# Optimization experiments

Hardware: AMD Instinct MI355X
Metric: run time of the kernel (lower is better)

The kernel has to match this reference:

```python
import math
import jax, jax.numpy as jnp
import numpy as np

B, S, D, H, F, L = 32, 512, 512, 8, 2048, 4
DH = D // H
ALPHA = 1.0
LN_EPS = 1e-12


def setup_inputs() -> dict:
    key = jax.random.key(0)
    ks = jax.random.split(key, 24)
    n = jax.random.normal
    inp = {
        "hidden_states": n(ks[0], (B, S, D), dtype=jnp.float32),
        "position_bias": n(ks[1], (1, H, S, S), dtype=jnp.float32) * 0.02,
        "timestamp": jnp.sort(jax.random.randint(ks[2], (B, S), 0, 10_000_000), axis=-1).astype(jnp.int64),
        # per-layer stacked BERT params
        "Wq": n(ks[3], (L, D, D), dtype=jnp.float32) * 0.02,
        "bq": jnp.zeros((L, D), dtype=jnp.float32),
        "Wk": n(ks[4], (L, D, D), dtype=jnp.float32) * 0.02,
        "bk": jnp.zeros((L, D), dtype=jnp.float32),
        "Wv": n(ks[5], (L, D, D), dtype=jnp.float32) * 0.02,
        "bv": jnp.zeros((L, D), dtype=jnp.float32),
        "Wo": n(ks[6], (L, D, D), dtype=jnp.float32) * 0.02,
        "bo": jnp.zeros((L, D), dtype=jnp.float32),
        "ln1_g": jnp.ones((L, D), dtype=jnp.float32),
        "ln1_b": jnp.zeros((L, D), dtype=jnp.float32),
        "Wi": n(ks[7], (L, D, F), dtype=jnp.float32) * 0.02,
        "bi": jnp.zeros((L, F), dtype=jnp.float32),
        "Wf": n(ks[8], (L, F, D), dtype=jnp.float32) * 0.02,
        "bf": jnp.zeros((L, D), dtype=jnp.float32),
        "ln2_g": jnp.ones((L, D), dtype=jnp.float32),
        "ln2_b": jnp.zeros((L, D), dtype=jnp.float32),
    }
    return inp


def _layernorm(x, g, b):
    mu = jnp.mean(x, axis=-1, keepdims=True)
    var = jnp.mean(jnp.square(x - mu), axis=-1, keepdims=True)
    return (x - mu) * jax.lax.rsqrt(var + LN_EPS) * g + b


def _encoder(hidden_states, position_bias, timestamp,
             Wq, bq, Wk, bk, Wv, bv, Wo, bo, ln1_g, ln1_b,
             Wi, bi, Wf, bf, ln2_g, ln2_b):
    b_, s_, d_ = hidden_states.shape
    # lag-time scale (encoder path: raw timestamps, minutes)
    t = timestamp.astype(jnp.float32)
    lag = (t[:, :, None] - t[:, None, :]) / (60.0 * 1000.0)  # [B,S,S]
    scale = (math.sqrt(DH) - ALPHA / (jnp.maximum(lag, 0.0) + 1.0) + ALPHA)[:, None, :, :]  # [B,1,S,S]

    x = hidden_states
    for l in range(L):
        q = (x @ Wq[l] + bq[l]).reshape(b_, s_, H, DH)
        k = (x @ Wk[l] + bk[l]).reshape(b_, s_, H, DH)
        v = (x @ Wv[l] + bv[l]).reshape(b_, s_, H, DH)
        scores = jnp.einsum('bqhd,bkhd->bhqk', q, k) / scale + position_bias
        probs = jax.nn.softmax(scores, axis=-1)
        ctx = jnp.einsum('bhqk,bkhd->bqhd', probs, v).reshape(b_, s_, d_)
        attn = _layernorm(ctx @ Wo[l] + bo[l] + x, ln1_g[l], ln1_b[l])
        h = jax.nn.gelu(attn @ Wi[l] + bi[l], approximate=False)
        x = _layernorm(h @ Wf[l] + bf[l] + attn, ln2_g[l], ln2_b[l])
    return x


def reference(hidden_states, position_bias, timestamp,
              Wq, bq, Wk, bk, Wv, bv, Wo, bo, ln1_g, ln1_b,
              Wi, bi, Wf, bf, ln2_g, ln2_b):
    return _encoder(hidden_states, position_bias, timestamp,
                    Wq, bq, Wk, bk, Wv, bv, Wo, bo, ln1_g, ln1_b,
                    Wi, bi, Wf, bf, ln2_g, ln2_b)
```

## Files before the change

kernel.cpp:

```cpp
#include <hip/hip_runtime.h>
#include <stdint.h>

#define B_ 32
#define S_ 512
#define D_ 512
#define H_ 8
#define F_ 2048
#define L_ 4
#define DH_ 64
#define M_ (B_*S_)

typedef unsigned short u16;
typedef float f32x4 __attribute__((ext_vector_type(4)));
typedef short bf16x8 __attribute__((ext_vector_type(8)));

__device__ __forceinline__ u16 f2b(float f) {
  unsigned u = __float_as_uint(f);
  u += 0x7FFFu + ((u >> 16) & 1u);
  return (u16)(u >> 16);
}
__device__ __forceinline__ float b2f(u16 u) {
  return __uint_as_float((unsigned)u << 16);
}
__device__ __forceinline__ void gld16(const void* g, void* l) {
  __builtin_amdgcn_global_load_lds((__attribute__((address_space(1))) void*)(void*)g,
                                   (__attribute__((address_space(3))) void*)l, 16, 0, 0);
}
__device__ __forceinline__ f32x4 mfma16(bf16x8 a, bf16x8 b, f32x4 c) {
  return __builtin_amdgcn_mfma_f32_16x16x32_bf16(a, b, c, 0, 0, 0);
}
__device__ __forceinline__ float gelu_fast(float x) {
  float z = 0.7978845608028654f * fmaf(0.044715f * x, x * x, x);
  float e = __expf(2.0f * z);
  float t = 1.0f - 2.0f * __builtin_amdgcn_rcpf(e + 1.0f);
  return 0.5f * x * (1.0f + t);
}

__global__ __launch_bounds__(256) void transpose_w(const float* __restrict__ in,
                                                   u16* __restrict__ out, int R, int C) {
  __shared__ float tile[32][33];
  const int l = blockIdx.z;
  in  += (size_t)l * R * C;
  out += (size_t)l * R * C;
  const int c0 = blockIdx.x * 32, r0 = blockIdx.y * 32;
  const int tx = threadIdx.x, ty = threadIdx.y;
#pragma unroll
  for (int k = 0; k < 4; k++)
    tile[ty + 8*k][tx] = in[(size_t)(r0 + ty + 8*k) * C + c0 + tx];
  __syncthreads();
#pragma unroll
  for (int k = 0; k < 4; k++)
    out[(size_t)(c0 + ty + 8*k) * R + r0 + tx] = f2b(tile[tx][ty + 8*k]);
}

__global__ __launch_bounds__(256) void prep_x(const float* __restrict__ h,
                                              u16* __restrict__ xb) {
  int i = blockIdx.x * 256 + threadIdx.x;
  float4 v = ((const float4*)h)[i];
  ushort4 u; u.x = f2b(v.x); u.y = f2b(v.y); u.z = f2b(v.z); u.w = f2b(v.w);
  ((ushort4*)xb)[i] = u;
}

__global__ __launch_bounds__(256) void prep_pb(const float* __restrict__ pb,
                                               u16* __restrict__ out) {
  int i = blockIdx.x * 256 + threadIdx.x;
  float4 v = ((const float4*)pb)[i];
  ushort4 o; o.x = f2b(v.x); o.y = f2b(v.y); o.z = f2b(v.z); o.w = f2b(v.w);
  ((ushort4*)out)[i] = o;
}

__device__ __forceinline__ void gemm_core(
    const u16* __restrict__ A, const u16* __restrict__ BT,
    const int N, const int K,
    const float* __restrict__ bias, u16* __restrict__ outb, const int epi)
{
  __shared__ u16 As[128*64];
  __shared__ u16 Bs[128*64];
  const int tid = threadIdx.x;
  const int wid = tid >> 6, lane = tid & 63;
  const int wm = (wid >> 1) * 64, wn = (wid & 1) * 64;
  const int lr = lane & 15, quad = lane >> 4;
  const int m0 = blockIdx.x * 128, n0 = blockIdx.y * 128;
  const int l7 = lane & 7, l3 = lane >> 3;
  const int cc = (l7 ^ l3) * 8;
  const int f8 = lr & 7;

  f32x4 acc[4][4];
#pragma unroll
  for (int i = 0; i < 4; i++)
#pragma unroll
    for (int j = 0; j < 4; j++) acc[i][j] = (f32x4){0.f, 0.f, 0.f, 0.f};

  const u16* Ag = A  + (size_t)(m0 + wid*16 + l3)*K + cc;
  const u16* Bg = BT + (size_t)(n0 + wid*16 + l3)*K + cc;
  u16* AsW = As + wid*1024;
  u16* BsW = Bs + wid*1024;

  for (int k0 = 0; k0 < K; k0 += 64) {
    gld16(Ag + k0,                 AsW);
    gld16(Ag + (size_t)8*K + k0,   AsW + 512);
    gld16(Ag + (size_t)64*K + k0,  AsW + 4096);
    gld16(Ag + (size_t)72*K + k0,  AsW + 4608);
    gld16(Bg + k0,                 BsW);
    gld16(Bg + (size_t)8*K + k0,   BsW + 512);
    gld16(Bg + (size_t)64*K + k0,  BsW + 4096);
    gld16(Bg + (size_t)72*K + k0,  BsW + 4608);
    __syncthreads();
#pragma unroll
    for (int kh = 0; kh < 2; kh++) {
      bf16x8 af[4], bfr[4];
#pragma unroll
      for (int i = 0; i < 4; i++)
        af[i]  = *(const bf16x8*)(As + (wm + i*16 + lr)*64 + (((kh*4 + quad) ^ f8) * 8));
#pragma unroll
      for (int j = 0; j < 4; j++)
        bfr[j] = *(const bf16x8*)(Bs + (wn + j*16 + lr)*64 + (((kh*4 + quad) ^ f8) * 8));
#pragma unroll
      for (int i = 0; i < 4; i++)
#pragma unroll
        for (int j = 0; j < 4; j++)
          acc[i][j] = mfma16(af[i], bfr[j], acc[i][j]);
    }
    __syncthreads();
  }

  float bn[4];
#pragma unroll
  for (int j = 0; j < 4; j++) bn[j] = bias[n0 + wn + j*16 + lr];

  if (epi == 3) {
#pragma unroll
    for (int i = 0; i < 4; i++) {
      const int m = m0 + wm + i*16 + quad*4;
      const int bb_ = m >> 9, sr = m & 511;
#pragma unroll
      for (int j = 0; j < 4; j++) {
        const int n = n0 + wn + j*16 + lr;
        const int hh = n >> 6, dd = n & 63;
        ushort4 o;
        o.x = f2b(acc[i][j][0] + bn[j]);
        o.y = f2b(acc[i][j][1] + bn[j]);
        o.z = f2b(acc[i][j][2] + bn[j]);
        o.w = f2b(acc[i][j][3] + bn[j]);
        *(ushort4*)(outb + (((size_t)((bb_*H_ + hh)*DH_ + dd)) << 9) + sr) = o;
      }
    }
  } else {
#pragma unroll
    for (int i = 0; i < 4; i++) {
#pragma unroll
      for (int r = 0; r < 4; r++) {
        const size_t m = (size_t)(m0 + wm + i*16 + quad*4 + r);
#pragma unroll
        for (int j = 0; j < 4; j++) {
          const int n = n0 + wn + j*16 + lr;
          float v = acc[i][j][r] + bn[j];
          if (epi == 2) v = gelu_fast(v);
          outb[m*N + n] = f2b(v);
        }
      }
    }
  }
}

__global__ __launch_bounds__(256) void gemm_kernel(
    const u16* A, const u16* BT, int N, int K,
    const float* bias, u16* outb, int epi)
{
  gemm_core(A, BT, N, K, bias, outb, epi);
}

__global__ __launch_bounds__(256) void gemm_qkv_kernel(
    const u16* A, const u16* BTq, size_t zstride, int K,
    const float* b0, const float* b1, const float* b2,
    u16* out0, u16* out1, u16* out2)
{
  const int z = blockIdx.z;
  const u16* BT = BTq + (size_t)z * zstride;
  const float* bias = (z == 0) ? b0 : (z == 1) ? b1 : b2;
  u16* outb = (z == 0) ? out0 : (z == 1) ? out1 : out2;
  gemm_core(A, BT, 512, K, bias, outb, (z == 2) ? 3 : 0);
}

__global__ __launch_bounds__(256) void gemm64_kernel(
    const u16* __restrict__ A, const u16* __restrict__ BT,
    const int N, const int K,
    const float* __restrict__ bias, const u16* __restrict__ resb,
    float* __restrict__ outf)
{
  __shared__ u16 As[64*64];
  __shared__ u16 Bs[128*64];
  const int tid = threadIdx.x;
  const int wid = tid >> 6, lane = tid & 63;
  const int wm = (wid >> 1) * 32, wn = (wid & 1) * 64;
  const int lr = lane & 15, quad = lane >> 4;
  const int m0 = blockIdx.x * 64, n0 = blockIdx.y * 128;
  const int l7 = lane & 7, l3 = lane >> 3;
  const int cc = (l7 ^ l3) * 8;
  const int f8 = lr & 7;

  f32x4 acc[2][4];
#pragma unroll
  for (int i = 0; i < 2; i++)
#pragma unroll
    for (int j = 0; j < 4; j++) acc[i][j] = (f32x4){0.f, 0.f, 0.f, 0.f};

  const u16* Ag = A  + (size_t)(m0 + wid*8 + l3)*K + cc;
  const u16* Bg = BT + (size_t)(n0 + wid*16 + l3)*K + cc;
  u16* AsW = As + wid*512;
  u16* BsW = Bs + wid*1024;

  for (int k0 = 0; k0 < K; k0 += 64) {
    gld16(Ag + k0,                AsW);
    gld16(Ag + (size_t)32*K + k0, AsW + 2048);
    gld16(Bg + k0,                 BsW);
    gld16(Bg + (size_t)8*K + k0,   BsW + 512);
    gld16(Bg + (size_t)64*K + k0,  BsW + 4096);
    gld16(Bg + (size_t)72*K + k0,  BsW + 4608);
    __syncthreads();
#pragma unroll
    for (int kh = 0; kh < 2; kh++) {
      bf16x8 af[2], bfr[4];
#pragma unroll
      for (int i = 0; i < 2; i++)
        af[i]  = *(const bf16x8*)(As + (wm + i*16 + lr)*64 + (((kh*4 + quad) ^ f8) * 8));
#pragma unroll
      for (int j = 0; j < 4; j++)
        bfr[j] = *(const bf16x8*)(Bs + (wn + j*16 + lr)*64 + (((kh*4 + quad) ^ f8) * 8));
#pragma unroll
      for (int i = 0; i < 2; i++)
#pragma unroll
        for (int j = 0; j < 4; j++)
          acc[i][j] = mfma16(af[i], bfr[j], acc[i][j]);
    }
    __syncthreads();
  }

  float bn[4];
#pragma unroll
  for (int j = 0; j < 4; j++) bn[j] = bias[n0 + wn + j*16 + lr];

#pragma unroll
  for (int i = 0; i < 2; i++) {
#pragma unroll
    for (int r = 0; r < 4; r++) {
      const size_t m = (size_t)(m0 + wm + i*16 + quad*4 + r);
#pragma unroll
      for (int j = 0; j < 4; j++) {
        const int n = n0 + wn + j*16 + lr;
        outf[m*N + n] = acc[i][j][r] + bn[j] + b2f(resb[m*N + n]);
      }
    }
  }
}

__global__ __launch_bounds__(256) void ln_kernel(
    const float* __restrict__ y, const float* __restrict__ g, const float* __restrict__ bta,
    float* __restrict__ outf, u16* __restrict__ outb)
{
  const int lane = threadIdx.x & 63;
  const int row = blockIdx.x*4 + (threadIdx.x >> 6);
  const float* yr = y + (size_t)row*D_ + lane*8;
  float4 a0 = *(const float4*)yr;
  float4 a1 = *(const float4*)(yr + 4);
  float v[8] = {a0.x, a0.y, a0.z, a0.w, a1.x, a1.y, a1.z, a1.w};
  float s = 0.f;
#pragma unroll
  for (int e = 0; e < 8; e++) s += v[e];
#pragma unroll
  for (int m = 1; m < 64; m <<= 1) s += __shfl_xor(s, m);
  const float mu = s * (1.0f/512.0f);
  float q = 0.f;
#pragma unroll
  for (int e = 0; e < 8; e++) { float d = v[e] - mu; q += d*d; }
#pragma unroll
  for (int m = 1; m < 64; m <<= 1) q += __shfl_xor(q, m);
  const float rs = rsqrtf(q * (1.0f/512.0f) + 1e-12f);
  float4 g0 = *(const float4*)(g + lane*8);
  float4 g1 = *(const float4*)(g + lane*8 + 4);
  float4 b0 = *(const float4*)(bta + lane*8);
  float4 b1 = *(const float4*)(bta + lane*8 + 4);
  float gg[8] = {g0.x, g0.y, g0.z, g0.w, g1.x, g1.y, g1.z, g1.w};
  float bb[8] = {b0.x, b0.y, b0.z, b0.w, b1.x, b1.y, b1.z, b1.w};
  float o[8];
#pragma unroll
  for (int e = 0; e < 8; e++) o[e] = (v[e] - mu) * rs * gg[e] + bb[e];
  if (outf) {
    float4 w0 = {o[0], o[1], o[2], o[3]}, w1 = {o[4], o[5], o[6], o[7]};
    *(float4*)(outf + (size_t)row*D_ + lane*8)     = w0;
    *(float4*)(outf + (size_t)row*D_ + lane*8 + 4) = w1;
  }
  ushort4 u0 = {f2b(o[0]), f2b(o[1]), f2b(o[2]), f2b(o[3])};
  ushort4 u1 = {f2b(o[4]), f2b(o[5]), f2b(o[6]), f2b(o[7])};
  *(ushort4*)(outb + (size_t)row*D_ + lane*8)     = u0;
  *(ushort4*)(outb + (size_t)row*D_ + lane*8 + 4) = u1;
}

__global__ __launch_bounds__(256, 4) void attn_kernel(
    const u16* __restrict__ qb, const u16* __restrict__ kb, const u16* __restrict__ vt,
    const u16* __restrict__ pb16, const int* __restrict__ ts, u16* __restrict__ cb)
{
  __shared__ u16 QPs[64*64];
  __shared__ u16 Ks[64*64], Vs[64*64], PBs[64*64];
  __shared__ float Tif[64], Tjf[64];
  const int b = blockIdx.x, it = blockIdx.y, h = blockIdx.z;
  const int i0 = it * 64;
  const int tid = threadIdx.x, wid = tid >> 6, lane = tid & 63;
  const int lr = lane & 15, quad = lane >> 4;
  const int l7 = lane & 7, l3 = lane >> 3;
  const int cc = (l7 ^ l3) * 8;
  const int f8 = lr & 7;
  const int rr = wid*8 + l3;

  const u16* qg  = qb + ((size_t)(b*S_ + i0))*D_ + h*DH_;
  const u16* kg  = kb + ((size_t)b*S_)*D_ + h*DH_;
  const u16* vg  = vt + ((size_t)(b*H_ + h)*DH_)*S_;
  const u16* pbg = pb16 + ((size_t)(h*S_ + i0))*S_;

  gld16(qg + (size_t)rr*D_ + cc,        QPs + wid*512);
  gld16(qg + (size_t)(rr+32)*D_ + cc,   QPs + 2048 + wid*512);
  if (tid < 64) Tif[tid] = (float)ts[b*S_ + i0 + tid] * (1.0f/60000.0f);
  __syncthreads();

  bf16x8 aq0 = *(const bf16x8*)(QPs + (wid*16 + lr)*64 + ((quad ^ f8) * 8));
  bf16x8 aq1 = *(const bf16x8*)(QPs + (wid*16 + lr)*64 + (((quad ^ f8) ^ 4) * 8));
  u16* Pw = QPs + wid*1024;

  float tis[4];
#pragma unroll
  for (int r = 0; r < 4; r++) tis[r] = Tif[wid*16 + quad*4 + r];

  f32x4 O[4]; float lacc[4];
#pragma unroll
  for (int dt = 0; dt < 4; dt++) O[dt] = (f32x4){0.f, 0.f, 0.f, 0.f};
#pragma unroll
  for (int r = 0; r < 4; r++) lacc[r] = 0.f;
  const int lrh = lr >> 3;

  for (int t8 = 0; t8 < 8; t8++) {
    const int j0 = t8 * 64;
    gld16(kg + (size_t)(j0+rr)*D_ + cc,      Ks + wid*512);
    gld16(kg + (size_t)(j0+rr+32)*D_ + cc,   Ks + 2048 + wid*512);
    gld16(vg + (size_t)rr*S_ + j0 + cc,      Vs + wid*512);
    gld16(vg + (size_t)(rr+32)*S_ + j0 + cc, Vs + 2048 + wid*512);
    gld16(pbg + (size_t)rr*S_ + j0 + cc,      PBs + wid*512);
    gld16(pbg + (size_t)(rr+32)*S_ + j0 + cc, PBs + 2048 + wid*512);
    if (tid < 64) Tjf[tid] = (float)ts[b*S_ + j0 + tid] * (1.0f/60000.0f);
    __syncthreads();

    f32x4 s[4];
#pragma unroll
    for (int jt = 0; jt < 4; jt++) {
      const u16* kr = Ks + (jt*16 + lr)*64;
      bf16x8 bk0 = *(const bf16x8*)(kr + ((quad ^ f8) * 8));
      bf16x8 bk1 = *(const bf16x8*)(kr + (((quad ^ f8) ^ 4) * 8));
      f32x4 z = (f32x4){0.f, 0.f, 0.f, 0.f};
      z = mfma16(aq0, bk0, z);
      z = mfma16(aq1, bk1, z);
      s[jt] = z;
    }
#pragma unroll
    for (int r = 0; r < 4; r++) {
      const int rowl = quad*4 + r;
      const int rbase = (wid*16 + rowl) * 64;
      const int r7 = rowl & 7;
      float pa = 0.f;
#pragma unroll
      for (int jt = 0; jt < 4; jt++) {
        const int idx = (((jt*2 + lrh) ^ r7) * 8) + l7;
        float lag = fmaxf(tis[r] - Tjf[idx], 0.0f);
        float inv = (lag + 1.0f) * __builtin_amdgcn_rcpf(fmaf(lag, 9.0f, 8.0f));
        float pbf = b2f(PBs[rbase + idx]);
        float p = __expf(fmaf(s[jt][r], inv, pbf));
        pa += p;
        Pw[rowl*64 + idx] = f2b(p);
      }
      lacc[r] += pa;
    }
    bf16x8 ap0 = *(const bf16x8*)(Pw + lr*64 + ((quad ^ f8) * 8));
    bf16x8 ap1 = *(const bf16x8*)(Pw + lr*64 + (((quad ^ f8) ^ 4) * 8));
#pragma unroll
    for (int dt = 0; dt < 4; dt++) {
      const u16* vr = Vs + (dt*16 + lr)*64;
      bf16x8 bv0 = *(const bf16x8*)(vr + ((quad ^ f8) * 8));
      bf16x8 bv1 = *(const bf16x8*)(vr + (((quad ^ f8) ^ 4) * 8));
      O[dt] = mfma16(ap0, bv0, O[dt]);
      O[dt] = mfma16(ap1, bv1, O[dt]);
    }
    __syncthreads();
  }

#pragma unroll
  for (int r = 0; r < 4; r++) {
    float sum = lacc[r];
#pragma unroll
    for (int m = 1; m < 16; m <<= 1) sum += __shfl_xor(sum, m);
    const float inv = __builtin_amdgcn_rcpf(sum);
    const size_t row = (size_t)(b*S_ + i0 + wid*16 + quad*4 + r);
#pragma unroll
    for (int dt = 0; dt < 4; dt++)
      cb[row*D_ + h*DH_ + dt*16 + lr] = f2b(O[dt][r] * inv);
  }
}

extern "C" void kernel_launch(void* const* d_in, const int* in_sizes, int n_in,
                              void* d_out, int out_size, void* d_ws, size_t ws_size,
                              hipStream_t stream)
{
  const float* hidden = (const float*)d_in[0];
  const float* pbias  = (const float*)d_in[1];
  const int*   ts     = (const int*)d_in[2];
  const float* Wq = (const float*)d_in[3];   const float* bq  = (const float*)d_in[4];
  const float* Wk = (const float*)d_in[5];   const float* bk  = (const float*)d_in[6];
  const float* Wv = (const float*)d_in[7];   const float* bv  = (const float*)d_in[8];
  const float* Wo = (const float*)d_in[9];   const float* bo  = (const float*)d_in[10];
  const float* l1g = (const float*)d_in[11]; const float* l1b = (const float*)d_in[12];
  const float* Wi = (const float*)d_in[13];  const float* bi  = (const float*)d_in[14];
  const float* Wf = (const float*)d_in[15];  const float* bfw = (const float*)d_in[16];
  const float* l2g = (const float*)d_in[17]; const float* l2b = (const float*)d_in[18];

  char* w = (char*)d_ws;
  u16* xb    = (u16*)w; w += (size_t)M_*D_*2;
  u16* qb    = (u16*)w; w += (size_t)M_*D_*2;
  u16* kbuf  = (u16*)w; w += (size_t)M_*D_*2;
  u16* vtw   = (u16*)w; w += (size_t)M_*D_*2;
  u16* cbuf  = (u16*)w; w += (size_t)M_*D_*2;
  u16* attnb = (u16*)w; w += (size_t)M_*D_*2;
  float* yf  = (float*)w; w += (size_t)M_*D_*4;
  u16* WqkvT = (u16*)w; w += (size_t)3*L_*D_*D_*2;
  u16* WoT   = (u16*)w; w += (size_t)L_*D_*D_*2;
  u16* WiT   = (u16*)w; w += (size_t)L_*D_*F_*2;
  u16* WfT   = (u16*)w; w += (size_t)L_*F_*D_*2;
  u16* pbb   = (u16*)w; w += (size_t)H_*S_*S_*2;
  u16* hb    = qb;

  float* x = (float*)d_out;

  const size_t WD = (size_t)D_*D_;
  const size_t WF = (size_t)D_*F_;
  dim3 tb(32, 8);

  transpose_w<<<dim3(16,16,L_), tb, 0, stream>>>(Wq, WqkvT,           D_, D_);
  transpose_w<<<dim3(16,16,L_), tb, 0, stream>>>(Wk, WqkvT + L_*WD,   D_, D_);
  transpose_w<<<dim3(16,16,L_), tb, 0, stream>>>(Wv, WqkvT + 2*L_*WD, D_, D_);
  transpose_w<<<dim3(16,16,L_), tb, 0, stream>>>(Wo, WoT,             D_, D_);
  transpose_w<<<dim3(64,16,L_), tb, 0, stream>>>(Wi, WiT,             D_, F_);
  transpose_w<<<dim3(16,64,L_), tb, 0, stream>>>(Wf, WfT,             F_, D_);
  prep_x<<<dim3(8192), dim3(256), 0, stream>>>(hidden, xb);
  prep_pb<<<dim3(H_*S_*S_/1024), dim3(256), 0, stream>>>(pbias, pbb);

  for (int l = 0; l < L_; l++) {
    gemm_qkv_kernel<<<dim3(128,4,3), dim3(256), 0, stream>>>(
        xb, WqkvT + l*WD, (size_t)L_*WD, D_,
        bq + l*D_, bk + l*D_, bv + l*D_, qb, kbuf, vtw);
    attn_kernel<<<dim3(B_,8,H_), dim3(256), 0, stream>>>(qb, kbuf, vtw, pbb, ts, cbuf);
    gemm64_kernel<<<dim3(256,4), dim3(256), 0, stream>>>(
        cbuf, WoT + l*WD, D_, D_, bo + l*D_, xb, yf);
    ln_kernel<<<dim3(4096), dim3(256), 0, stream>>>(yf, l1g + l*D_, l1b + l*D_,
                                                    (float*)nullptr, attnb);
    gemm_kernel<<<dim3(128,16), dim3(256), 0, stream>>>(
        attnb, WiT + l*WF, F_, D_, bi + l*F_, hb, 2);
    gemm64_kernel<<<dim3(256,4), dim3(256), 0, stream>>>(
        hb, WfT + l*WF, D_, F_, bfw + l*D_, attnb, yf);
    ln_kernel<<<dim3(4096), dim3(256), 0, stream>>>(yf, l2g + l*D_, l2b + l*D_,
                                                    (l == 3) ? x : (float*)nullptr, xb);
  }
}
```

Before: 1.106 ms.

## Precompute lag-scale table once and switch softmax exponent to exp2

Adds a prep kernel that computes the per-batch [S,S] inverse lag-scale factor (pre-multiplied by log2e) once and stores it as 16-bit fixed point. The attention kernel then loads this tile into shared memory along with K/V/bias, and no longer recomputes lag and reciprocal per score. Position bias is also pre-scaled by log2e so the kernel can call exp2 directly. This trades per-element ALU work for extra global traffic (a B*S*S u16 table read by every head in every layer), and the fixed-point encoding loses some precision.

```diff
diff --git a/kernel.cpp b/kernel.cpp
--- a/kernel.cpp
+++ b/kernel.cpp
@@ -36,6 +36,8 @@
   return 0.5f * x * (1.0f + t);
 }
 
+#define LOG2E 1.4426950408889634f
+
 __global__ __launch_bounds__(256) void transpose_w(const float* __restrict__ in,
                                                    u16* __restrict__ out, int R, int C) {
   __shared__ float tile[32][33];
@@ -65,8 +67,33 @@
                                                u16* __restrict__ out) {
   int i = blockIdx.x * 256 + threadIdx.x;
   float4 v = ((const float4*)pb)[i];
-  ushort4 o; o.x = f2b(v.x); o.y = f2b(v.y); o.z = f2b(v.z); o.w = f2b(v.w);
+  ushort4 o;
+  o.x = f2b(v.x * LOG2E); o.y = f2b(v.y * LOG2E);
+  o.z = f2b(v.z * LOG2E); o.w = f2b(v.w * LOG2E);
   ((ushort4*)out)[i] = o;
+}
+
+__global__ __launch_bounds__(256) void prep_inv(const int* __restrict__ ts,
+                                                u16* __restrict__ invb) {
+  const int b  = blockIdx.x >> 7;
+  const int rg = blockIdx.x & 127;
+  const int wid = threadIdx.x >> 6, lane = threadIdx.x & 63;
+  const int i = rg * 4 + wid;
+  const float ti = (float)ts[b*S_ + i];
+  int4 t0 = *(const int4*)(ts + b*S_ + lane*8);
+  int4 t1 = *(const int4*)(ts + b*S_ + lane*8 + 4);
+  int tj[8] = {t0.x, t0.y, t0.z, t0.w, t1.x, t1.y, t1.z, t1.w};
+  u16 o[8];
+#pragma unroll
+  for (int e = 0; e < 8; e++) {
+    float lag = fmaxf((ti - (float)tj[e]) * (1.0f/60000.0f), 0.0f);
+    float iv  = (lag + 1.0f) * __builtin_amdgcn_rcpf(fmaf(lag, 9.0f, 8.0f)) * LOG2E;
+    o[e] = (u16)(int)rintf((iv - 0.16f) * 524288.0f);
+  }
+  ushort4 w0 = {o[0], o[1], o[2], o[3]}, w1 = {o[4], o[5], o[6], o[7]};
+  u16* out = invb + (((size_t)(b*S_ + i)) << 9) + lane*8;
+  *(ushort4*)out       = w0;
+  *(ushort4*)(out + 4) = w1;
 }
 
 __device__ __forceinline__ void gemm_core(
@@ -298,11 +325,10 @@
 
 __global__ __launch_bounds__(256, 4) void attn_kernel(
     const u16* __restrict__ qb, const u16* __restrict__ kb, const u16* __restrict__ vt,
-    const u16* __restrict__ pb16, const int* __restrict__ ts, u16* __restrict__ cb)
+    const u16* __restrict__ pb16, const u16* __restrict__ invb, u16* __restrict__ cb)
 {
   __shared__ u16 QPs[64*64];
-  __shared__ u16 Ks[64*64], Vs[64*64], PBs[64*64];
-  __shared__ float Tif[64], Tjf[64];
+  __shared__ u16 Ks[64*64], Vs[64*64], PBs[64*64], INVs[64*64];
   const int b = blockIdx.x, it = blockIdx.y, h = blockIdx.z;
   const int i0 = it * 64;
   const int tid = threadIdx.x, wid = tid >> 6, lane = tid & 63;
@@ -316,20 +342,16 @@
   const u16* kg  = kb + ((size_t)b*S_)*D_ + h*DH_;
   const u16* vg  = vt + ((size_t)(b*H_ + h)*DH_)*S_;
   const u16* pbg = pb16 + ((size_t)(h*S_ + i0))*S_;
+  const u16* ivg = invb + ((size_t)(b*S_ + i0))*S_;
 
   gld16(qg + (size_t)rr*D_ + cc,        QPs + wid*512);
   gld16(qg + (size_t)(rr+32)*D_ + cc,   QPs + 2048 + wid*512);
-  if (tid < 64) Tif[tid] = (float)ts[b*S_ + i0 + tid] * (1.0f/60000.0f);
   __syncthreads();
 
   bf16x8 aq0 = *(const bf16x8*)(QPs + (wid*16 + lr)*64 + ((quad ^ f8) * 8));
   bf16x8 aq1 = *(const bf16x8*)(QPs + (wid*16 + lr)*64 + (((quad ^ f8) ^ 4) * 8));
   u16* Pw = QPs + wid*1024;
 
-  float tis[4];
-#pragma unroll
-  for (int r = 0; r < 4; r++) tis[r] = Tif[wid*16 + quad*4 + r];
-
   f32x4 O[4]; float lacc[4];
 #pragma unroll
   for (int dt = 0; dt < 4; dt++) O[dt] = (f32x4){0.f, 0.f, 0.f, 0.f};
@@ -339,13 +361,14 @@
 
   for (int t8 = 0; t8 < 8; t8++) {
     const int j0 = t8 * 64;
-    gld16(kg + (size_t)(j0+rr)*D_ + cc,      Ks + wid*512);
-    gld16(kg + (size_t)(j0+rr+32)*D_ + cc,   Ks + 2048 + wid*512);
-    gld16(vg + (size_t)rr*S_ + j0 + cc,      Vs + wid*512);
-    gld16(vg + (size_t)(rr+32)*S_ + j0 + cc, Vs + 2048 + wid*512);
-    gld16(pbg + (size_t)rr*S_ + j0 + cc,      PBs + wid*512);
-    gld16(pbg + (size_t)(rr+32)*S_ + j0 + cc, PBs + 2048 + wid*512);
-    if (tid < 64) Tjf[tid] = (float)ts[b*S_ + j0 + tid] * (1.0f/60000.0f);
+    gld16(kg + (size_t)(j0+rr)*D_ + cc,       Ks   + wid*512);
+    gld16(kg + (size_t)(j0+rr+32)*D_ + cc,    Ks   + 2048 + wid*512);
+    gld16(vg + (size_t)rr*S_ + j0 + cc,       Vs   + wid*512);
+    gld16(vg + (size_t)(rr+32)*S_ + j0 + cc,  Vs   + 2048 + wid*512);
+    gld16(pbg + (size_t)rr*S_ + j0 + cc,      PBs  + wid*512);
+    gld16(pbg + (size_t)(rr+32)*S_ + j0 + cc, PBs  + 2048 + wid*512);
+    gld16(ivg + (size_t)rr*S_ + j0 + cc,      INVs + wid*512);
+    gld16(ivg + (size_t)(rr+32)*S_ + j0 + cc, INVs + 2048 + wid*512);
     __syncthreads();
 
     f32x4 s[4];
@@ -368,10 +391,9 @@
 #pragma unroll
       for (int jt = 0; jt < 4; jt++) {
         const int idx = (((jt*2 + lrh) ^ r7) * 8) + l7;
-        float lag = fmaxf(tis[r] - Tjf[idx], 0.0f);
-        float inv = (lag + 1.0f) * __builtin_amdgcn_rcpf(fmaf(lag, 9.0f, 8.0f));
+        float iv  = fmaf((float)INVs[rbase + idx], 0x1p-19f, 0.16f);
         float pbf = b2f(PBs[rbase + idx]);
-        float p = __expf(fmaf(s[jt][r], inv, pbf));
+        float p = __builtin_amdgcn_exp2f(fmaf(s[jt][r], iv, pbf));
         pa += p;
         Pw[rowl*64 + idx] = f2b(p);
       }
@@ -432,6 +454,7 @@
   u16* WiT   = (u16*)w; w += (size_t)L_*D_*F_*2;
   u16* WfT   = (u16*)w; w += (size_t)L_*F_*D_*2;
   u16* pbb   = (u16*)w; w += (size_t)H_*S_*S_*2;
+  u16* invb  = (u16*)w; w += (size_t)B_*S_*S_*2;
   u16* hb    = qb;
 
   float* x = (float*)d_out;
@@ -448,12 +471,13 @@
   transpose_w<<<dim3(16,64,L_), tb, 0, stream>>>(Wf, WfT,             F_, D_);
   prep_x<<<dim3(8192), dim3(256), 0, stream>>>(hidden, xb);
   prep_pb<<<dim3(H_*S_*S_/1024), dim3(256), 0, stream>>>(pbias, pbb);
+  prep_inv<<<dim3(B_*S_/4), dim3(256), 0, stream>>>(ts, invb);
 
   for (int l = 0; l < L_; l++) {
     gemm_qkv_kernel<<<dim3(128,4,3), dim3(256), 0, stream>>>(
         xb, WqkvT + l*WD, (size_t)L_*WD, D_,
         bq + l*D_, bk + l*D_, bv + l*D_, qb, kbuf, vtw);
-    attn_kernel<<<dim3(B_,8,H_), dim3(256), 0, stream>>>(qb, kbuf, vtw, pbb, ts, cbuf);
+    attn_kernel<<<dim3(B_,8,H_), dim3(256), 0, stream>>>(qb, kbuf, vtw, pbb, invb, cbuf);
     gemm64_kernel<<<dim3(256,4), dim3(256), 0, stream>>>(
         cbuf, WoT + l*WD, D_, D_, bo + l*D_, xb, yf);
     ln_kernel<<<dim3(4096), dim3(256), 0, stream>>>(yf, l1g + l*D_, l1b + l*D_,
```

Measured after the change: 1.059 ms. 1.04x faster.
